# Kernel tuning notes

Hardware: AMD Instinct MI355X
Metric: run time of the kernel (lower is better)

## Reference

```python
import jax, jax.numpy as jnp
from jax import lax
import numpy as np

B, T, D, H, K = 16, 1024, 1024, 1024, 2


def setup_inputs() -> dict:
    key = jax.random.key(0)
    k1, k2 = jax.random.split(key, 2)
    inputs = jax.random.normal(k1, (B, T, D), dtype=jnp.float32)
    # small init so tanh/sigmoid gates are not saturated
    conv_w = jax.random.normal(k2, (3 * H, D, K), dtype=jnp.float32) * 0.02
    conv_b = jnp.zeros((3 * H,), dtype=jnp.float32)
    return {"inputs": inputs, "conv_w": conv_w, "conv_b": conv_b, "layer_idx": 0}


def _qrnn_forward(inputs, conv_w, conv_b):
    k = conv_w.shape[-1]
    h = conv_w.shape[0] // 3
    # causal conv1d: pad (k-1) on the left of the time axis
    x = jnp.transpose(inputs, (0, 2, 1))                 # [B, D, T]
    x = jnp.pad(x, ((0, 0), (0, 0), (k - 1, 0)))         # [B, D, T+k-1]
    gates = lax.conv_general_dilated(
        x, conv_w, window_strides=(1,), padding="VALID",
        dimension_numbers=("NCH", "OIH", "NCH"))         # [B, 3H, T]
    gates = jnp.transpose(gates, (0, 2, 1)) + conv_b     # [B, T, 3H]
    Z = jnp.tanh(gates[..., :h])
    F = jax.nn.sigmoid(gates[..., h:2 * h])
    O = jax.nn.sigmoid(gates[..., 2 * h:])

    # fo-pooling recurrence: c_t = f_t * c_{t-1} + (1 - f_t) * z_t, c_0 = 0
    def step(c, zf):
        z, f = zf
        c_ = f * c + (1.0 - f) * z
        return c_, c_

    c0 = jnp.zeros((Z.shape[0], h), dtype=Z.dtype)
    zT = jnp.transpose(Z, (1, 0, 2))                     # [T, B, H]
    fT = jnp.transpose(F, (1, 0, 2))
    _, cT = lax.scan(step, c0, (zT, fT))                 # [T, B, H]
    c_time = jnp.transpose(cT, (1, 0, 2))                # [B, T, H]
    h_time = O * c_time
    return c_time, h_time


def reference(inputs, conv_w, conv_b, layer_idx):
    # layer_idx=0 with state=None, memory=None: no conv_linear memory term,
    # no attention, zero initial cell state.
    return _qrnn_forward(inputs, conv_w, conv_b)
```

## Files before the change

### kernel.cpp

```cpp
#include <hip/hip_runtime.h>

#define BB 16
#define TT 1024
#define DD 1024
#define HH 1024
#define NN 3072
#define KK 2048
#define MM (BB * TT)
#define TP (TT + 1)
#define NCH 32
#define TC  32
#define PLANE (1u << 24)

typedef __attribute__((ext_vector_type(8))) short short8;
typedef __attribute__((ext_vector_type(4))) float float4v;

__device__ __forceinline__ unsigned short f2bf(float f) {
    unsigned int u = __float_as_uint(f);
    u += 0x7fffu + ((u >> 16) & 1u);
    return (unsigned short)(u >> 16);
}
__device__ __forceinline__ float bf2f(unsigned short s) {
    return __uint_as_float(((unsigned int)s) << 16);
}

__device__ __forceinline__ void gload_lds16(const unsigned short* g, unsigned short* l) {
    __builtin_amdgcn_global_load_lds(
        (const __attribute__((address_space(1))) unsigned int*)(g),
        (__attribute__((address_space(3))) unsigned int*)(l),
        16, 0, 0);
}

__global__ __launch_bounds__(256) void pack_x_kernel(const float* __restrict__ x,
                                                     unsigned short* __restrict__ xpad) {
    int i = blockIdx.x * 256 + threadIdx.x;
    int total = BB * TP * (DD / 4);
    if (i >= total) return;
    int d4  = i & (DD / 4 - 1);
    int row = i >> 8;
    int b  = row / TP;
    int tp = row - b * TP;
    float4 v = make_float4(0.f, 0.f, 0.f, 0.f);
    if (tp > 0)
        v = ((const float4*)x)[(((size_t)(b * TT + tp - 1)) << 8) + d4];
    ushort4 r4;
    r4.x = f2bf(v.x); r4.y = f2bf(v.y); r4.z = f2bf(v.z); r4.w = f2bf(v.w);
    *(ushort4*)(xpad + (((size_t)row) << 10) + (d4 << 2)) = r4;
}

__global__ __launch_bounds__(256) void pack_w_kernel(const float* __restrict__ w,
                                                     unsigned short* __restrict__ Bt) {
    int i = blockIdx.x * 256 + threadIdx.x;
    if (i >= NN * DD) return;
    int n = i >> 10, d = i & 1023;
    float2 v = ((const float2*)w)[i];
    Bt[(size_t)n * KK + d]       = f2bf(v.x);
    Bt[(size_t)n * KK + DD + d]  = f2bf(v.y);
}

__global__ __launch_bounds__(256) void gemm_gates_kernel(const unsigned short* __restrict__ xpad,
                                                         const unsigned short* __restrict__ Bt,
                                                         const float* __restrict__ bias,
                                                         unsigned short* __restrict__ zT) {
    __shared__ unsigned short smem[16384];
    unsigned short* As = smem;
    unsigned short* Bs = smem + 4096;

    const int tid  = threadIdx.x;
    const int lane = tid & 63;
    const int wave = tid >> 6;
    const int m0 = blockIdx.x * 128;
    const int n0 = blockIdx.y * 128;

    const int bidx = m0 >> 10;
    const int t0   = m0 & 1023;
    const unsigned short* aBase = xpad + (((size_t)(bidx * TP + t0)) << 10);

    const int msub = (wave & 1) << 6;
    const int nsub = (wave >> 1) << 6;
    const int mrow = lane & 15;
    const int quad = lane >> 4;
    const int csw = (quad ^ ((mrow >> 1) & 3)) << 3;

    float4v acc[4][4];
#pragma unroll
    for (int i = 0; i < 4; i++)
#pragma unroll
        for (int j = 0; j < 4; j++) acc[i][j] = (float4v)0.0f;

    for (int kb = 0; kb < KK / 32; ++kb) {
        const int tap = kb >> 5;
        const int kd0 = (kb & 31) << 5;
#pragma unroll
        for (int q = 0; q < 2; ++q) {
            int ci = q * 256 + tid;
            int r  = ci >> 2;
            int cs = (((ci & 3) ^ ((r >> 1) & 3)) << 3);
            gload_lds16(aBase + (((size_t)(r + tap)) << 10) + kd0 + cs, As + ci * 8);
            gload_lds16(Bt + (size_t)(n0 + r) * KK + (kb << 5) + cs, Bs + ci * 8);
        }
        __syncthreads();

        short8 af[4], bf[4];
#pragma unroll
        for (int i = 0; i < 4; i++) {
            af[i] = *(const short8*)(As + (msub + i * 16 + mrow) * 32 + csw);
            bf[i] = *(const short8*)(Bs + (nsub + i * 16 + mrow) * 32 + csw);
        }
#pragma unroll
        for (int i = 0; i < 4; i++)
#pragma unroll
            for (int j = 0; j < 4; j++)
                acc[i][j] = __builtin_amdgcn_mfma_f32_16x16x32_bf16(af[i], bf[j], acc[i][j], 0, 0, 0);
        __syncthreads();
    }
    unsigned short* Ts = smem;

    const bool isZ = (n0 < HH);
#pragma unroll
    for (int j = 0; j < 4; j++) {
        int nloc = nsub + j * 16 + mrow;
        float bv = bias[n0 + nloc];
#pragma unroll
        for (int i = 0; i < 4; i++) {
            int mcol = msub + i * 16 + (quad << 2);
            unsigned int d0, d1;
            {
                float v0 = acc[i][j][0] + bv, v1 = acc[i][j][1] + bv;
                float v2 = acc[i][j][2] + bv, v3 = acc[i][j][3] + bv;
                float g0, g1, g2, g3;
                if (isZ) {
                    g0 = 2.0f * __builtin_amdgcn_rcpf(1.0f + __expf(-2.0f * v0)) - 1.0f;
                    g1 = 2.0f * __builtin_amdgcn_rcpf(1.0f + __expf(-2.0f * v1)) - 1.0f;
                    g2 = 2.0f * __builtin_amdgcn_rcpf(1.0f + __expf(-2.0f * v2)) - 1.0f;
                    g3 = 2.0f * __builtin_amdgcn_rcpf(1.0f + __expf(-2.0f * v3)) - 1.0f;
                } else {
                    g0 = __builtin_amdgcn_rcpf(1.0f + __expf(-v0));
                    g1 = __builtin_amdgcn_rcpf(1.0f + __expf(-v1));
                    g2 = __builtin_amdgcn_rcpf(1.0f + __expf(-v2));
                    g3 = __builtin_amdgcn_rcpf(1.0f + __expf(-v3));
                }
                d0 = (unsigned int)f2bf(g0) | ((unsigned int)f2bf(g1) << 16);
                d1 = (unsigned int)f2bf(g2) | ((unsigned int)f2bf(g3) << 16);
            }
            int chunk = (mcol >> 3) ^ (nloc & 7);
            int el = nloc * 128 + (chunk << 3) + (mcol & 7);
            *(uint2*)(Ts + el) = make_uint2(d0, d1);
        }
    }
    __syncthreads();

    const int rl = tid & 15;
    const int rg = tid >> 4;
    const int gate = n0 >> 10;
    unsigned short* plane = zT + ((size_t)gate << 24);
#pragma unroll
    for (int p = 0; p < 8; p++) {
        int np = (p << 4) + rg;
        int lchunk = rl ^ (np & 7);
        short8 vv = *(const short8*)(Ts + np * 128 + (lchunk << 3));
        int h = (n0 & 1023) + np;
        size_t dst = ((((size_t)((bidx << 10) | h)) << 10) | (unsigned)(t0 + (rl << 3)));
        *(short8*)(plane + dst) = vv;
    }
}


__global__ __launch_bounds__(256) void scan_summary_kernel(const unsigned short* __restrict__ zT,
                                                           float* __restrict__ P,
                                                           float* __restrict__ S) {
    int g = blockIdx.x * 256 + threadIdx.x;
    int h = g & 1023;
    int b = (g >> 10) & 15;
    int j = g >> 14;
    const unsigned short* zp = zT + ((((size_t)((b << 10) | h)) << 10) + j * TC);
    const unsigned short* fp = zp + PLANE;
    short8 zv[4], fv[4];
#pragma unroll
    for (int q = 0; q < 4; ++q) {
        zv[q] = *(const short8*)(zp + q * 8);
        fv[q] = *(const short8*)(fp + q * 8);
    }
    float c = 0.f, pr = 1.f;
#pragma unroll
    for (int q = 0; q < 4; ++q)
#pragma unroll
        for (int k = 0; k < 8; ++k) {
            float z = bf2f((unsigned short)zv[q][k]);
            float f = bf2f((unsigned short)fv[q][k]);
            c = fmaf(f, c, (1.0f - f) * z);
            pr *= f;
        }
    int o = (j << 14) | (b << 10) | h;
    P[o] = pr;
    S[o] = c;
}

__global__ __launch_bounds__(256) void scan_prefix_kernel(const float* __restrict__ P,
                                                          const float* __restrict__ S,
                                                          float* __restrict__ Cin) {
    int idx = blockIdx.x * 256 + threadIdx.x;
    float c = 0.f;
#pragma unroll
    for (int j = 0; j < NCH; ++j) {
        int o = (j << 14) + idx;
        Cin[o] = c;
        c = fmaf(P[o], c, S[o]);
    }
}

__global__ __launch_bounds__(256) void scan_apply_kernel(const unsigned short* __restrict__ zT,
                                                         const float* __restrict__ Cin,
                                                         float* __restrict__ out) {
    int g = blockIdx.x * 256 + threadIdx.x;
    int h = g & 1023;
    int b = (g >> 10) & 15;
    int j = g >> 14;
    const unsigned short* zp = zT + ((((size_t)((b << 10) | h)) << 10) + j * TC);
    const unsigned short* fp = zp + PLANE;
    const unsigned short* op = zp + 2 * (size_t)PLANE;
    short8 zv[4], fv[4], ov[4];
#pragma unroll
    for (int q = 0; q < 4; ++q) {
        zv[q] = *(const short8*)(zp + q * 8);
        fv[q] = *(const short8*)(fp + q * 8);
        ov[q] = *(const short8*)(op + q * 8);
    }
    float c = Cin[(j << 14) | (b << 10) | h];
    float* cbase = out + ((((size_t)((b << 10) | (j * TC))) << 10) | h);
#pragma unroll
    for (int q = 0; q < 4; ++q)
#pragma unroll
        for (int k = 0; k < 8; ++k) {
            float z = bf2f((unsigned short)zv[q][k]);
            float f = bf2f((unsigned short)fv[q][k]);
            float o = bf2f((unsigned short)ov[q][k]);
            c = fmaf(f, c, (1.0f - f) * z);
            float* cp = cbase + (((size_t)(q * 8 + k)) << 10);
            cp[0] = c;
            cp[(size_t)1 << 24] = o * c;
        }
}

extern "C" void kernel_launch(void* const* d_in, const int* in_sizes, int n_in,
                              void* d_out, int out_size, void* d_ws, size_t ws_size,
                              hipStream_t stream) {
    const float* x    = (const float*)d_in[0];
    const float* w    = (const float*)d_in[1];
    const float* bias = (const float*)d_in[2];
    float* out = (float*)d_out;

    char* ws = (char*)d_ws;
    const size_t xpad_bytes = (size_t)BB * TP * DD * 2;
    const size_t btw_bytes  = (size_t)NN * KK * 2;
    unsigned short* xpad = (unsigned short*)ws;
    unsigned short* Btw  = (unsigned short*)(ws + xpad_bytes);
    unsigned short* zT   = (unsigned short*)(ws + xpad_bytes + btw_bytes);
    float* P   = (float*)ws;
    float* S   = (float*)(ws + (size_t)MM * NCH * 4);
    float* Cin = (float*)(ws + (size_t)MM * NCH * 8);

    {
        int total = BB * TP * (DD / 4);
        pack_x_kernel<<<(total + 255) / 256, 256, 0, stream>>>(x, xpad);
    }
    {
        int total = NN * DD;
        pack_w_kernel<<<(total + 255) / 256, 256, 0, stream>>>(w, Btw);
    }
    {
        dim3 grid(MM / 128, NN / 128);
        gemm_gates_kernel<<<grid, 256, 0, stream>>>(xpad, Btw, bias, zT);
    }
    scan_summary_kernel<<<MM * NCH / 256, 256, 0, stream>>>(zT, P, S);
    scan_prefix_kernel<<<MM / 256, 256, 0, stream>>>(P, S, Cin);
    scan_apply_kernel<<<MM * NCH / 256, 256, 0, stream>>>(zT, Cin, out);
}
```

Before: 497.1 us.

## Rewrite gate GEMM with 256x256 tiles, double-buffered LDS and async prefetch

The gate GEMM moves from 128x128 tiles with a single LDS buffer and 32-wide K steps to 256x256 tiles, 512 threads, 64-wide K steps and double-buffered LDS. Each K tile is prefetched by direct global-to-LDS loads while MFMAs run on the previous tile, with s_setprio around the MFMA bursts and a new XOR swizzle. The goal is to raise arithmetic intensity and hide global memory latency. The cost is 128 KB of dynamic LDS per block, higher register pressure from 32 accumulators per wave, and a grid of only 768 blocks.

New measurement: 459.3 us. 7.6% less time.

```diff
diff --git a/kernel.cpp b/kernel.cpp
--- a/kernel.cpp
+++ b/kernel.cpp
@@ -58,109 +58,155 @@
     Bt[(size_t)n * KK + DD + d]  = f2bf(v.y);
 }
 
-__global__ __launch_bounds__(256) void gemm_gates_kernel(const unsigned short* __restrict__ xpad,
-                                                         const unsigned short* __restrict__ Bt,
-                                                         const float* __restrict__ bias,
-                                                         unsigned short* __restrict__ zT) {
-    __shared__ unsigned short smem[16384];
-    unsigned short* As = smem;
-    unsigned short* Bs = smem + 4096;
+
+#define VMCNT0 asm volatile("s_waitcnt vmcnt(0)" ::: "memory")
+#define BARRIER_F() do { __builtin_amdgcn_s_barrier(); asm volatile("" ::: "memory"); } while (0)
+
+#define STAGE_TILE(ASN, BSN, KT) do {                                          \
+    const int tap_ = (KT) >> 4;                                                \
+    const size_t aoff_ = aSrc + (((size_t)tap_) << 10) + (((KT) & 15) << 6);   \
+    const size_t boff_ = bSrc + (((size_t)(KT)) << 6);                         \
+    gload_lds16(xpad + aoff_,                 (ASN) + ldsStage);               \
+    gload_lds16(xpad + aoff_ + (64u << 10),   (ASN) + ldsStage + 4096);        \
+    gload_lds16(xpad + aoff_ + (128u << 10),  (ASN) + ldsStage + 8192);        \
+    gload_lds16(xpad + aoff_ + (192u << 10),  (ASN) + ldsStage + 12288);       \
+    gload_lds16(Btw + boff_,                  (BSN) + ldsStage);               \
+    gload_lds16(Btw + boff_ + (64u << 11),    (BSN) + ldsStage + 4096);        \
+    gload_lds16(Btw + boff_ + (128u << 11),   (BSN) + ldsStage + 8192);        \
+    gload_lds16(Btw + boff_ + (192u << 11),   (BSN) + ldsStage + 12288);       \
+} while (0)
+
+#define PHASE_A(ASC, Q, TAIL) do {                                             \
+    const unsigned short* ap_ = (ASC) + aRowRd + ((Q) << 11);                  \
+    short8 af0k0 = *(const short8*)(ap_ + pch0);                               \
+    short8 af0k1 = *(const short8*)(ap_ + pch1);                               \
+    short8 af1k0 = *(const short8*)(ap_ + 1024 + pch0);                        \
+    short8 af1k1 = *(const short8*)(ap_ + 1024 + pch1);                        \
+    BARRIER_F();                                                               \
+    __builtin_amdgcn_s_setprio(1);                                             \
+    _Pragma("unroll")                                                          \
+    for (int ng = 0; ng < 4; ++ng) {                                           \
+        acc[(Q)*2][ng]   = __builtin_amdgcn_mfma_f32_16x16x32_bf16(af0k0, bfr[ng][0], acc[(Q)*2][ng], 0, 0, 0);   \
+        acc[(Q)*2][ng]   = __builtin_amdgcn_mfma_f32_16x16x32_bf16(af0k1, bfr[ng][1], acc[(Q)*2][ng], 0, 0, 0);   \
+        acc[(Q)*2+1][ng] = __builtin_amdgcn_mfma_f32_16x16x32_bf16(af1k0, bfr[ng][0], acc[(Q)*2+1][ng], 0, 0, 0); \
+        acc[(Q)*2+1][ng] = __builtin_amdgcn_mfma_f32_16x16x32_bf16(af1k1, bfr[ng][1], acc[(Q)*2+1][ng], 0, 0, 0); \
+    }                                                                          \
+    __builtin_amdgcn_s_setprio(0);                                             \
+    TAIL;                                                                      \
+    BARRIER_F();                                                               \
+} while (0)
+
+#define TILE(ASC, BSC, ASN, BSN, KTN, DOSTAGE) do {                            \
+    short8 bfr[4][2];                                                          \
+    if (DOSTAGE) { STAGE_TILE(ASN, BSN, KTN); }                                \
+    _Pragma("unroll")                                                          \
+    for (int ng = 0; ng < 4; ++ng) {                                           \
+        bfr[ng][0] = *(const short8*)((BSC) + bRowRd + (ng << 10) + pch0);     \
+        bfr[ng][1] = *(const short8*)((BSC) + bRowRd + (ng << 10) + pch1);     \
+    }                                                                          \
+    PHASE_A(ASC, 0, ((void)0));                                                \
+    PHASE_A(ASC, 1, ((void)0));                                                \
+    PHASE_A(ASC, 2, ((void)0));                                                \
+    PHASE_A(ASC, 3, if (DOSTAGE) { VMCNT0; });                                 \
+} while (0)
+
+__global__ __launch_bounds__(512, 2) void gemm_gates_kernel(const unsigned short* __restrict__ xpad,
+                                                            const unsigned short* __restrict__ Btw,
+                                                            const float* __restrict__ bias,
+                                                            unsigned short* __restrict__ zT) {
+    extern __shared__ unsigned short lds[];
+    unsigned short* As0 = lds;
+    unsigned short* As1 = lds + 16384;
+    unsigned short* Bs0 = lds + 32768;
+    unsigned short* Bs1 = lds + 49152;
 
     const int tid  = threadIdx.x;
     const int lane = tid & 63;
-    const int wave = tid >> 6;
-    const int m0 = blockIdx.x * 128;
-    const int n0 = blockIdx.y * 128;
-
+    const int w    = tid >> 6;
+    const int wm   = w >> 2;
+    const int wn   = w & 3;
+    const int mrow = lane & 15;
+    const int quad = lane >> 4;
+
+    const int m0 = blockIdx.x << 8;
+    const int n0 = blockIdx.y << 8;
     const int bidx = m0 >> 10;
     const int t0   = m0 & 1023;
-    const unsigned short* aBase = xpad + (((size_t)(bidx * TP + t0)) << 10);
-
-    const int msub = (wave & 1) << 6;
-    const int nsub = (wave >> 1) << 6;
-    const int mrow = lane & 15;
-    const int quad = lane >> 4;
-    const int csw = (quad ^ ((mrow >> 1) & 3)) << 3;
-
-    float4v acc[4][4];
-#pragma unroll
-    for (int i = 0; i < 4; i++)
-#pragma unroll
-        for (int j = 0; j < 4; j++) acc[i][j] = (float4v)0.0f;
-
-    for (int kb = 0; kb < KK / 32; ++kb) {
-        const int tap = kb >> 5;
-        const int kd0 = (kb & 31) << 5;
-#pragma unroll
-        for (int q = 0; q < 2; ++q) {
-            int ci = q * 256 + tid;
-            int r  = ci >> 2;
-            int cs = (((ci & 3) ^ ((r >> 1) & 3)) << 3);
-            gload_lds16(aBase + (((size_t)(r + tap)) << 10) + kd0 + cs, As + ci * 8);
-            gload_lds16(Bt + (size_t)(n0 + r) * KK + (kb << 5) + cs, Bs + ci * 8);
+
+    const int rr  = tid >> 3;
+    const int cc8 = (((tid & 7) ^ (rr & 7)) << 3);
+    const size_t aSrc = (((size_t)(bidx * TP + t0 + rr)) << 10) + cc8;
+    const size_t bSrc = (((size_t)(n0 + rr)) << 11) + cc8;
+    const int ldsStage = (rr << 6) + ((tid & 7) << 3);
+
+    const int pch0 = ((quad ^ (lane & 7)) << 3);
+    const int pch1 = (((4 | quad) ^ (lane & 7)) << 3);
+    const int aRowRd = ((wm << 7) + mrow) << 6;
+    const int bRowRd = ((wn << 6) + mrow) << 6;
+
+    float4v acc[8][4];
+#pragma unroll
+    for (int i = 0; i < 8; ++i)
+#pragma unroll
+        for (int j = 0; j < 4; ++j) acc[i][j] = (float4v)0.0f;
+
+    STAGE_TILE(As0, Bs0, 0);
+    VMCNT0;
+    BARRIER_F();
+
+#pragma unroll 1
+    for (int jt = 0; jt < 30; jt += 2) {
+        TILE(As0, Bs0, As1, Bs1, jt + 1, 1);
+        TILE(As1, Bs1, As0, Bs0, jt + 2, 1);
+    }
+    TILE(As0, Bs0, As1, Bs1, 31, 1);
+    TILE(As1, Bs1, As0, Bs0, 0, 0);
+
+    unsigned short* Ts = lds;
+    const bool isZ = (n0 < HH);
+    float bv[4];
+#pragma unroll
+    for (int ng = 0; ng < 4; ++ng) bv[ng] = bias[n0 + (wn << 6) + (ng << 4) + mrow];
+
+#pragma unroll
+    for (int g = 0; g < 8; ++g) {
+#pragma unroll
+        for (int ng = 0; ng < 4; ++ng) {
+            const int nloc = (wn << 6) + (ng << 4) + mrow;
+            const int m0l  = (wm << 7) + (g << 4) + (quad << 2);
+            float v0 = acc[g][ng][0] + bv[ng];
+            float v1 = acc[g][ng][1] + bv[ng];
+            float v2 = acc[g][ng][2] + bv[ng];
+            float v3 = acc[g][ng][3] + bv[ng];
+            float g0, g1, g2, g3;
+            if (isZ) {
+                g0 = 2.0f * __builtin_amdgcn_rcpf(1.0f + __expf(-2.0f * v0)) - 1.0f;
+                g1 = 2.0f * __builtin_amdgcn_rcpf(1.0f + __expf(-2.0f * v1)) - 1.0f;
+                g2 = 2.0f * __builtin_amdgcn_rcpf(1.0f + __expf(-2.0f * v2)) - 1.0f;
+                g3 = 2.0f * __builtin_amdgcn_rcpf(1.0f + __expf(-2.0f * v3)) - 1.0f;
+            } else {
+                g0 = __builtin_amdgcn_rcpf(1.0f + __expf(-v0));
+                g1 = __builtin_amdgcn_rcpf(1.0f + __expf(-v1));
+                g2 = __builtin_amdgcn_rcpf(1.0f + __expf(-v2));
+                g3 = __builtin_amdgcn_rcpf(1.0f + __expf(-v3));
+            }
+            unsigned int d0 = (unsigned int)f2bf(g0) | ((unsigned int)f2bf(g1) << 16);
+            unsigned int d1 = (unsigned int)f2bf(g2) | ((unsigned int)f2bf(g3) << 16);
+            const int chunk = (m0l >> 3) ^ (nloc & 31);
+            *(uint2*)(Ts + nloc * 256 + (chunk << 3) + (m0l & 7)) = make_uint2(d0, d1);
         }
-        __syncthreads();
-
-        short8 af[4], bf[4];
-#pragma unroll
-        for (int i = 0; i < 4; i++) {
-            af[i] = *(const short8*)(As + (msub + i * 16 + mrow) * 32 + csw);
-            bf[i] = *(const short8*)(Bs + (nsub + i * 16 + mrow) * 32 + csw);
-        }
-#pragma unroll
-        for (int i = 0; i < 4; i++)
-#pragma unroll
-            for (int j = 0; j < 4; j++)
-                acc[i][j] = __builtin_amdgcn_mfma_f32_16x16x32_bf16(af[i], bf[j], acc[i][j], 0, 0, 0);
-        __syncthreads();
-    }
-    unsigned short* Ts = smem;
-
-    const bool isZ = (n0 < HH);
-#pragma unroll
-    for (int j = 0; j < 4; j++) {
-        int nloc = nsub + j * 16 + mrow;
-        float bv = bias[n0 + nloc];
-#pragma unroll
-        for (int i = 0; i < 4; i++) {
-            int mcol = msub + i * 16 + (quad << 2);
-            unsigned int d0, d1;
-            {
-                float v0 = acc[i][j][0] + bv, v1 = acc[i][j][1] + bv;
-                float v2 = acc[i][j][2] + bv, v3 = acc[i][j][3] + bv;
-                float g0, g1, g2, g3;
-                if (isZ) {
-                    g0 = 2.0f * __builtin_amdgcn_rcpf(1.0f + __expf(-2.0f * v0)) - 1.0f;
-                    g1 = 2.0f * __builtin_amdgcn_rcpf(1.0f + __expf(-2.0f * v1)) - 1.0f;
-                    g2 = 2.0f * __builtin_amdgcn_rcpf(1.0f + __expf(-2.0f * v2)) - 1.0f;
-                    g3 = 2.0f * __builtin_amdgcn_rcpf(1.0f + __expf(-2.0f * v3)) - 1.0f;
-                } else {
-                    g0 = __builtin_amdgcn_rcpf(1.0f + __expf(-v0));
-                    g1 = __builtin_amdgcn_rcpf(1.0f + __expf(-v1));
-                    g2 = __builtin_amdgcn_rcpf(1.0f + __expf(-v2));
-                    g3 = __builtin_amdgcn_rcpf(1.0f + __expf(-v3));
-                }
-                d0 = (unsigned int)f2bf(g0) | ((unsigned int)f2bf(g1) << 16);
-                d1 = (unsigned int)f2bf(g2) | ((unsigned int)f2bf(g3) << 16);
-            }
-            int chunk = (mcol >> 3) ^ (nloc & 7);
-            int el = nloc * 128 + (chunk << 3) + (mcol & 7);
-            *(uint2*)(Ts + el) = make_uint2(d0, d1);
-        }
     }
     __syncthreads();
 
-    const int rl = tid & 15;
-    const int rg = tid >> 4;
     const int gate = n0 >> 10;
     unsigned short* plane = zT + ((size_t)gate << 24);
-#pragma unroll
-    for (int p = 0; p < 8; p++) {
-        int np = (p << 4) + rg;
-        int lchunk = rl ^ (np & 7);
-        short8 vv = *(const short8*)(Ts + np * 128 + (lchunk << 3));
-        int h = (n0 & 1023) + np;
-        size_t dst = ((((size_t)((bidx << 10) | h)) << 10) | (unsigned)(t0 + (rl << 3)));
+    const int cl = lane & 31;
+#pragma unroll
+    for (int p = 0; p < 16; ++p) {
+        const int np = (p << 4) + (tid >> 5);
+        short8 vv = *(const short8*)(Ts + np * 256 + ((cl ^ (np & 31)) << 3));
+        const int h = (n0 & 1023) + np;
+        const size_t dst = ((((size_t)((bidx << 10) | h)) << 10) | (unsigned)(t0 + (cl << 3)));
         *(short8*)(plane + dst) = vv;
     }
 }
@@ -269,8 +315,14 @@
         pack_w_kernel<<<(total + 255) / 256, 256, 0, stream>>>(w, Btw);
     }
     {
-        dim3 grid(MM / 128, NN / 128);
-        gemm_gates_kernel<<<grid, 256, 0, stream>>>(xpad, Btw, bias, zT);
+        static int gemm_attr_done = 0;
+        if (!gemm_attr_done) {
+            (void)hipFuncSetAttribute((const void*)gemm_gates_kernel,
+                                      hipFuncAttributeMaxDynamicSharedMemorySize, 131072);
+            gemm_attr_done = 1;
+        }
+        dim3 grid(MM / 256, NN / 256);
+        gemm_gates_kernel<<<grid, 512, 131072, stream>>>(xpad, Btw, bias, zT);
     }
     scan_summary_kernel<<<MM * NCH / 256, 256, 0, stream>>>(zT, P, S);
     scan_prefix_kernel<<<MM / 256, 256, 0, stream>>>(P, S, Cin);
```
